# Performance work log

Measured on AMD Instinct MI355X. Metric: run time of the kernel, lower is better.

The kernel has to match this reference:

```python
import jax, jax.numpy as jnp
import numpy as np

BIT_SHIFT = 4
PROJECT = True
DIMS = [4096, 4096, 4096, 4096]
BATCH = 8192


def ternarize(w):
    # Ternary weight quantization {-1,0,+1} with straight-through estimator.
    q = jnp.clip(jnp.round(w), -1.0, 1.0)
    return w + jax.lax.stop_gradient(q - w)


def binarize(x):
    # Binary projection sign(x) with hardtanh straight-through estimator.
    c = jnp.clip(x, -1.0, 1.0)
    return c + jax.lax.stop_gradient(jnp.sign(x) - c)


def tern_bin_layer(x, w):
    # Ternary-weight matmul followed by bit-shift scaling (divide by 2**BIT_SHIFT),
    # then optional binary projection of the activation.
    scale = 1.0 / (1 << BIT_SHIFT)
    y = jnp.matmul(x, ternarize(w)) * scale
    if PROJECT:
        y = binarize(y)
    return y


def setup_inputs() -> dict:
    key = jax.random.key(0)
    ks = jax.random.split(key, 4)
    x = jax.random.normal(ks[0], (BATCH, DIMS[0]), dtype=jnp.float32)
    # Latent float weights; ternarized inside the layer.
    W0 = jax.random.normal(ks[1], (DIMS[0], DIMS[1]), dtype=jnp.float32) * 0.7
    W1 = jax.random.normal(ks[2], (DIMS[1], DIMS[2]), dtype=jnp.float32) * 0.7
    W2 = jax.random.normal(ks[3], (DIMS[2], DIMS[3]), dtype=jnp.float32) * 0.7
    return {"x": x, "W0": W0, "W1": W1, "W2": W2}


def reference(x, W0, W1, W2):
    h = tern_bin_layer(x, W0)
    h = tern_bin_layer(h, W1)
    h = tern_bin_layer(h, W2)
    return h
```

## Files before the change

kernel.cpp:

```cpp
#include <hip/hip_runtime.h>
#include <stdint.h>

#define MDIM 8192
#define KDIM 4096
#define NDIM 4096

typedef int i32x4 __attribute__((ext_vector_type(4)));

__device__ __forceinline__ void gl2lds16(const void* g, void* l) {
  __builtin_amdgcn_global_load_lds(
      (const __attribute__((address_space(1))) void*)(uintptr_t)(g),
      (__attribute__((address_space(3))) void*)(uintptr_t)(l), 16, 0, 0);
}

__global__ __launch_bounds__(256) void k_tern(const float* __restrict__ W,
                                              int8_t* __restrict__ Qt) {
  __shared__ int8_t t[64][65];
  const int n0 = blockIdx.x * 64;
  const int k0 = blockIdx.y * 64;
  const int tid = threadIdx.x;
  const int c = tid & 63;
  const int r0 = tid >> 6;
#pragma unroll
  for (int i = 0; i < 16; ++i) {
    int r = (i << 2) + r0;
    float w = W[(size_t)(k0 + r) * NDIM + (n0 + c)];
    float q = fminf(1.f, fmaxf(-1.f, rintf(w)));
    t[r][c] = (int8_t)(int)q;
  }
  __syncthreads();
#pragma unroll
  for (int i = 0; i < 16; ++i) {
    int r = (i << 2) + r0;
    Qt[(size_t)(n0 + r) * KDIM + (k0 + c)] = t[c][r];
  }
}

__global__ __launch_bounds__(256) void k_quant(const float* __restrict__ x,
                                               int8_t* __restrict__ dig) {
  const size_t P = (size_t)MDIM * KDIM;
  size_t i = ((size_t)blockIdx.x * 256 + threadIdx.x) * 4;
  float4 v = *(const float4*)(x + i);
  float f[4] = {v.x, v.y, v.z, v.w};
  int8_t dd[4][4];
#pragma unroll
  for (int j = 0; j < 4; ++j) {
    long long s = __double2ll_rn((double)f[j] * 268435456.0);
    int8_t d0 = (int8_t)s; s = (s - d0) >> 8;
    int8_t d1 = (int8_t)s; s = (s - d1) >> 8;
    int8_t d2 = (int8_t)s; s = (s - d2) >> 8;
    int8_t d3 = (int8_t)s;
    dd[0][j] = d0; dd[1][j] = d1; dd[2][j] = d2; dd[3][j] = d3;
  }
#pragma unroll
  for (int p = 0; p < 4; ++p) {
    char4 c4; c4.x = dd[p][0]; c4.y = dd[p][1]; c4.z = dd[p][2]; c4.w = dd[p][3];
    *(char4*)(dig + p * P + i) = c4;
  }
}

__global__ __launch_bounds__(512) void k_gemm_l1(const int8_t* __restrict__ dig,
                                                 const int8_t* __restrict__ Qt,
                                                 int8_t* __restrict__ h) {
  __shared__ __align__(16) int8_t As[4][64][128];
  __shared__ __align__(16) int8_t Bs[128][128];
  const int tid = threadIdx.x;
  const int w = tid >> 6, l = tid & 63;
  const size_t P = (size_t)MDIM * KDIM;

  const int nwg = gridDim.x;
  const int wg = (blockIdx.x & 7) * (nwg >> 3) + (blockIdx.x >> 3);
  const int NB = NDIM / 128;
  const int mb = wg / NB, nb = wg % NB;

  const int srow = tid >> 3;
  const int sswz = (tid & 7) ^ (srow & 7);
  const int8_t* a_src = dig + (size_t)(mb * 64 + srow) * KDIM + sswz * 16;
  const int8_t* b_src0 = Qt + (size_t)(nb * 128 + srow) * KDIM + sswz * 16;
  const int8_t* b_src1 = b_src0 + (size_t)64 * KDIM;
  int8_t* a_dst = &As[0][0][0] + w * 1024;
  int8_t* b_dst = &Bs[0][0] + w * 1024;

  i32x4 acc[4][2][2];
#pragma unroll
  for (int p = 0; p < 4; ++p)
#pragma unroll
    for (int mi = 0; mi < 2; ++mi)
#pragma unroll
      for (int ni = 0; ni < 2; ++ni) acc[p][mi][ni] = (i32x4){0, 0, 0, 0};

  const int wr = (w >> 2) * 32;
  const int wc = (w & 3) * 32;

  for (int kk = 0; kk < KDIM; kk += 128) {
#pragma unroll
    for (int p = 0; p < 4; ++p) gl2lds16(a_src + p * P + kk, a_dst + p * 8192);
    gl2lds16(b_src0 + kk, b_dst);
    gl2lds16(b_src1 + kk, b_dst + 8192);
    __syncthreads();
#pragma unroll
    for (int ki = 0; ki < 2; ++ki) {
      const int kg = ki * 4 + (l >> 4);
      i32x4 b[2];
#pragma unroll
      for (int ni = 0; ni < 2; ++ni) {
        int nr = wc + ni * 16 + (l & 15);
        b[ni] = *(const i32x4*)&Bs[nr][(kg ^ (nr & 7)) * 16];
      }
#pragma unroll
      for (int p = 0; p < 4; ++p)
#pragma unroll
        for (int mi = 0; mi < 2; ++mi) {
          int ar = wr + mi * 16 + (l & 15);
          i32x4 a = *(const i32x4*)&As[p][ar][(kg ^ (ar & 7)) * 16];
#pragma unroll
          for (int ni = 0; ni < 2; ++ni)
            acc[p][mi][ni] =
                __builtin_amdgcn_mfma_i32_16x16x64_i8(a, b[ni], acc[p][mi][ni], 0, 0, 0);
        }
    }
    __syncthreads();
  }

  const int mbase = mb * 64 + wr + ((l >> 4) << 2);
  const int nbase = nb * 128 + wc + (l & 15);
#pragma unroll
  for (int mi = 0; mi < 2; ++mi)
#pragma unroll
    for (int ni = 0; ni < 2; ++ni)
#pragma unroll
      for (int j = 0; j < 4; ++j) {
        int s0 = acc[0][mi][ni][j], s1 = acc[1][mi][ni][j];
        int s2 = acc[2][mi][ni][j], s3 = acc[3][mi][ni][j];
        double d = (double)(s3 * 256 + s2) * 65536.0 + (double)(s1 * 256 + s0);
        int sg = (d > 0.0) - (d < 0.0);
        h[(size_t)(mbase + mi * 16 + j) * NDIM + (nbase + ni * 16)] = (int8_t)sg;
      }
}

template <int F32OUT>
__global__ __launch_bounds__(512) void k_gemm_bin(const int8_t* __restrict__ A,
                                                  const int8_t* __restrict__ Qt,
                                                  void* __restrict__ outp) {
  __shared__ __align__(16) int8_t As[128][128];
  __shared__ __align__(16) int8_t Bs[128][128];
  const int tid = threadIdx.x;
  const int w = tid >> 6, l = tid & 63;

  const int nwg = gridDim.x;
  const int wg = (blockIdx.x & 7) * (nwg >> 3) + (blockIdx.x >> 3);
  const int NB = NDIM / 128;
  const int mb = wg / NB, nb = wg % NB;

  const int srow = tid >> 3;
  const int sswz = (tid & 7) ^ (srow & 7);
  const int8_t* a0 = A + (size_t)(mb * 128 + srow) * KDIM + sswz * 16;
  const int8_t* a1 = a0 + (size_t)64 * KDIM;
  const int8_t* b0 = Qt + (size_t)(nb * 128 + srow) * KDIM + sswz * 16;
  const int8_t* b1 = b0 + (size_t)64 * KDIM;
  int8_t* a_dst = &As[0][0] + w * 1024;
  int8_t* b_dst = &Bs[0][0] + w * 1024;

  i32x4 acc[4][2];
#pragma unroll
  for (int mi = 0; mi < 4; ++mi)
#pragma unroll
    for (int ni = 0; ni < 2; ++ni) acc[mi][ni] = (i32x4){0, 0, 0, 0};

  const int wr = (w >> 2) * 64, wc = (w & 3) * 32;

  for (int kk = 0; kk < KDIM; kk += 128) {
    gl2lds16(a0 + kk, a_dst);
    gl2lds16(a1 + kk, a_dst + 8192);
    gl2lds16(b0 + kk, b_dst);
    gl2lds16(b1 + kk, b_dst + 8192);
    __syncthreads();
#pragma unroll
    for (int ki = 0; ki < 2; ++ki) {
      const int kg = ki * 4 + (l >> 4);
      i32x4 b[2];
#pragma unroll
      for (int ni = 0; ni < 2; ++ni) {
        int nr = wc + ni * 16 + (l & 15);
        b[ni] = *(const i32x4*)&Bs[nr][(kg ^ (nr & 7)) * 16];
      }
#pragma unroll
      for (int mi = 0; mi < 4; ++mi) {
        int ar = wr + mi * 16 + (l & 15);
        i32x4 a = *(const i32x4*)&As[ar][(kg ^ (ar & 7)) * 16];
#pragma unroll
        for (int ni = 0; ni < 2; ++ni)
          acc[mi][ni] = __builtin_amdgcn_mfma_i32_16x16x64_i8(a, b[ni], acc[mi][ni], 0, 0, 0);
      }
    }
    __syncthreads();
  }

  const int mbase = mb * 128 + wr + ((l >> 4) << 2);
  const int nbase = nb * 128 + wc + (l & 15);
#pragma unroll
  for (int mi = 0; mi < 4; ++mi)
#pragma unroll
    for (int ni = 0; ni < 2; ++ni)
#pragma unroll
      for (int j = 0; j < 4; ++j) {
        int s = acc[mi][ni][j];
        int sg = (s > 0) - (s < 0);
        size_t off = (size_t)(mbase + mi * 16 + j) * NDIM + (nbase + ni * 16);
        if (F32OUT)
          ((float*)outp)[off] = (float)sg;
        else
          ((int8_t*)outp)[off] = (int8_t)sg;
      }
}

extern "C" void kernel_launch(void* const* d_in, const int* in_sizes, int n_in,
                              void* d_out, int out_size, void* d_ws, size_t ws_size,
                              hipStream_t stream) {
  (void)in_sizes; (void)n_in; (void)out_size; (void)ws_size;
  const float* x  = (const float*)d_in[0];
  const float* W0 = (const float*)d_in[1];
  const float* W1 = (const float*)d_in[2];
  const float* W2 = (const float*)d_in[3];
  float* out = (float*)d_out;

  const size_t QB = (size_t)KDIM * NDIM;
  const size_t HB = (size_t)MDIM * NDIM;
  int8_t* Qt0 = (int8_t*)d_ws;
  int8_t* Qt1 = Qt0 + QB;
  int8_t* Qt2 = Qt1 + QB;
  int8_t* h0  = Qt2 + QB;
  int8_t* h1  = h0 + HB;
  int8_t* dig = (int8_t*)d_out;

  dim3 tgrid(NDIM / 64, KDIM / 64);
  k_tern<<<tgrid, 256, 0, stream>>>(W0, Qt0);
  k_tern<<<tgrid, 256, 0, stream>>>(W1, Qt1);
  k_tern<<<tgrid, 256, 0, stream>>>(W2, Qt2);
  k_quant<<<((size_t)MDIM * KDIM) / 1024, 256, 0, stream>>>(x, dig);
  k_gemm_l1<<<(MDIM / 64) * (NDIM / 128), 512, 0, stream>>>(dig, Qt0, h0);
  k_gemm_bin<0><<<(MDIM / 128) * (NDIM / 128), 512, 0, stream>>>(h0, Qt1, h1);
  k_gemm_bin<1><<<(MDIM / 128) * (NDIM / 128), 512, 0, stream>>>(h1, Qt2, out);
}
```

Before: 882.1 us.

## Use three int8 digit planes for layer 1 with exact fixup for near-zero outputs

Layer one now splits the fp32 input into three int8 digit planes at a lower fixed-point scale instead of four, so the first GEMM does a quarter less MFMA work and A-tile traffic. Outputs whose reconstructed sum lies within a small margin of zero are recorded through an atomic counter into a flag list. A new fixup kernel then recomputes those entries in double precision from the original fp32 input to keep the sign exact. This adds atomics, an extra launch and per-flag dot products, and drops correction silently if the flag buffer overflows.

```diff
diff --git a/kernel.cpp b/kernel.cpp
--- a/kernel.cpp
+++ b/kernel.cpp
@@ -4,6 +4,7 @@
 #define MDIM 8192
 #define KDIM 4096
 #define NDIM 4096
+#define MAXFLAGS (2 * 1024 * 1024)
 
 typedef int i32x4 __attribute__((ext_vector_type(4)));
 
@@ -42,27 +43,32 @@
   size_t i = ((size_t)blockIdx.x * 256 + threadIdx.x) * 4;
   float4 v = *(const float4*)(x + i);
   float f[4] = {v.x, v.y, v.z, v.w};
-  int8_t dd[4][4];
+  int8_t dd[3][4];
 #pragma unroll
   for (int j = 0; j < 4; ++j) {
-    long long s = __double2ll_rn((double)f[j] * 268435456.0);
+    long long s = __double2ll_rn((double)f[j] * 524288.0);
     int8_t d0 = (int8_t)s; s = (s - d0) >> 8;
     int8_t d1 = (int8_t)s; s = (s - d1) >> 8;
-    int8_t d2 = (int8_t)s; s = (s - d2) >> 8;
-    int8_t d3 = (int8_t)s;
-    dd[0][j] = d0; dd[1][j] = d1; dd[2][j] = d2; dd[3][j] = d3;
-  }
-#pragma unroll
-  for (int p = 0; p < 4; ++p) {
+    int8_t d2 = (int8_t)s;
+    dd[0][j] = d0; dd[1][j] = d1; dd[2][j] = d2;
+  }
+#pragma unroll
+  for (int p = 0; p < 3; ++p) {
     char4 c4; c4.x = dd[p][0]; c4.y = dd[p][1]; c4.z = dd[p][2]; c4.w = dd[p][3];
     *(char4*)(dig + p * P + i) = c4;
   }
 }
 
+__global__ void k_zero(int* c) {
+  if (threadIdx.x == 0 && blockIdx.x == 0) *c = 0;
+}
+
 __global__ __launch_bounds__(512) void k_gemm_l1(const int8_t* __restrict__ dig,
                                                  const int8_t* __restrict__ Qt,
-                                                 int8_t* __restrict__ h) {
-  __shared__ __align__(16) int8_t As[4][64][128];
+                                                 int8_t* __restrict__ h,
+                                                 int* __restrict__ cnt,
+                                                 int2* __restrict__ flags) {
+  __shared__ __align__(16) int8_t As[3][64][128];
   __shared__ __align__(16) int8_t Bs[128][128];
   const int tid = threadIdx.x;
   const int w = tid >> 6, l = tid & 63;
@@ -81,9 +87,9 @@
   int8_t* a_dst = &As[0][0][0] + w * 1024;
   int8_t* b_dst = &Bs[0][0] + w * 1024;
 
-  i32x4 acc[4][2][2];
-#pragma unroll
-  for (int p = 0; p < 4; ++p)
+  i32x4 acc[3][2][2];
+#pragma unroll
+  for (int p = 0; p < 3; ++p)
 #pragma unroll
     for (int mi = 0; mi < 2; ++mi)
 #pragma unroll
@@ -94,7 +100,7 @@
 
   for (int kk = 0; kk < KDIM; kk += 128) {
 #pragma unroll
-    for (int p = 0; p < 4; ++p) gl2lds16(a_src + p * P + kk, a_dst + p * 8192);
+    for (int p = 0; p < 3; ++p) gl2lds16(a_src + p * P + kk, a_dst + p * 8192);
     gl2lds16(b_src0 + kk, b_dst);
     gl2lds16(b_src1 + kk, b_dst + 8192);
     __syncthreads();
@@ -108,7 +114,7 @@
         b[ni] = *(const i32x4*)&Bs[nr][(kg ^ (nr & 7)) * 16];
       }
 #pragma unroll
-      for (int p = 0; p < 4; ++p)
+      for (int p = 0; p < 3; ++p)
 #pragma unroll
         for (int mi = 0; mi < 2; ++mi) {
           int ar = wr + mi * 16 + (l & 15);
@@ -131,11 +137,47 @@
 #pragma unroll
       for (int j = 0; j < 4; ++j) {
         int s0 = acc[0][mi][ni][j], s1 = acc[1][mi][ni][j];
-        int s2 = acc[2][mi][ni][j], s3 = acc[3][mi][ni][j];
-        double d = (double)(s3 * 256 + s2) * 65536.0 + (double)(s1 * 256 + s0);
+        int s2 = acc[2][mi][ni][j];
+        double d = ((double)s2 * 256.0 + (double)s1) * 256.0 + (double)s0;
         int sg = (d > 0.0) - (d < 0.0);
-        h[(size_t)(mbase + mi * 16 + j) * NDIM + (nbase + ni * 16)] = (int8_t)sg;
-      }
+        int row = mbase + mi * 16 + j;
+        int col = nbase + ni * 16;
+        h[(size_t)row * NDIM + col] = (int8_t)sg;
+        if (fabs(d) <= 2048.0) {
+          int idx = atomicAdd(cnt, 1);
+          if (idx < MAXFLAGS) flags[idx] = make_int2(row, col);
+        }
+      }
+}
+
+__global__ __launch_bounds__(256) void k_fixup(const float* __restrict__ x,
+                                               const int8_t* __restrict__ Qt,
+                                               const int* __restrict__ cnt,
+                                               const int2* __restrict__ flags,
+                                               int8_t* __restrict__ h) {
+  __shared__ double red[256];
+  int n = *cnt;
+  if (n > MAXFLAGS) n = MAXFLAGS;
+  for (int i = blockIdx.x; i < n; i += gridDim.x) {
+    int2 rc = flags[i];
+    const float* xr = x + (size_t)rc.x * KDIM;
+    const int8_t* qr = Qt + (size_t)rc.y * KDIM;
+    double s = 0.0;
+    for (int k = threadIdx.x; k < KDIM; k += 256)
+      s += (double)xr[k] * (double)qr[k];
+    red[threadIdx.x] = s;
+    __syncthreads();
+#pragma unroll
+    for (int st = 128; st > 0; st >>= 1) {
+      if (threadIdx.x < st) red[threadIdx.x] += red[threadIdx.x + st];
+      __syncthreads();
+    }
+    if (threadIdx.x == 0) {
+      double d = red[0];
+      h[(size_t)rc.x * NDIM + rc.y] = (int8_t)((d > 0.0) - (d < 0.0));
+    }
+    __syncthreads();
+  }
 }
 
 template <int F32OUT>
@@ -231,14 +273,19 @@
   int8_t* Qt2 = Qt1 + QB;
   int8_t* h0  = Qt2 + QB;
   int8_t* h1  = h0 + HB;
+
   int8_t* dig = (int8_t*)d_out;
+  int2* flags = (int2*)((char*)d_out + 3 * HB);
+  int* cnt = (int*)((char*)d_out + 3 * HB + (size_t)MAXFLAGS * 8);
 
   dim3 tgrid(NDIM / 64, KDIM / 64);
   k_tern<<<tgrid, 256, 0, stream>>>(W0, Qt0);
   k_tern<<<tgrid, 256, 0, stream>>>(W1, Qt1);
   k_tern<<<tgrid, 256, 0, stream>>>(W2, Qt2);
   k_quant<<<((size_t)MDIM * KDIM) / 1024, 256, 0, stream>>>(x, dig);
-  k_gemm_l1<<<(MDIM / 64) * (NDIM / 128), 512, 0, stream>>>(dig, Qt0, h0);
+  k_zero<<<1, 64, 0, stream>>>(cnt);
+  k_gemm_l1<<<(MDIM / 64) * (NDIM / 128), 512, 0, stream>>>(dig, Qt0, h0, cnt, flags);
+  k_fixup<<<512, 256, 0, stream>>>(x, Qt0, cnt, flags, h0);
   k_gemm_bin<0><<<(MDIM / 128) * (NDIM / 128), 512, 0, stream>>>(h0, Qt1, h1);
   k_gemm_bin<1><<<(MDIM / 128) * (NDIM / 128), 512, 0, stream>>>(h1, Qt2, out);
 }
```

Measured after the change: 795.3 us. 9.8% less time.
